# Optimization experiments

Measured on AMD Instinct MI355X. Metric: run time of the kernel, lower is better.

The kernel has to match this reference:

```python
import jax, jax.numpy as jnp
import numpy as np

N, E, H, HEADS, HD, L = 4096, 65536, 128, 4, 32, 4
NF, GF, EF, B = 16, 8, 4, 1


def _ln(x, g, b, eps=1e-5):
    mu = x.mean(-1, keepdims=True)
    v = ((x - mu) ** 2).mean(-1, keepdims=True)
    return (x - mu) * jax.lax.rsqrt(v + eps) * g + b


def _lin(x, W, b=None):
    y = x @ W.T
    return y if b is None else y + b


def _gelu(x):
    return jax.nn.gelu(x, approximate=False)


def setup_inputs() -> dict:
    key = jax.random.key(0)
    ks = iter(jax.random.split(key, 64))
    def rn(shape, s=0.05):
        return jax.random.normal(next(ks), shape, jnp.float32) * s
    inp = {}
    inp['x'] = jax.random.normal(next(ks), (N, NF), jnp.float32)
    inp['edge_index'] = jax.random.randint(next(ks), (2, E), 0, N, dtype=jnp.int32)
    inp['edge_attr'] = jax.random.normal(next(ks), (E, EF), jnp.float32)
    inp['u'] = jax.random.normal(next(ks), (1, GF), jnp.float32)
    inp['acting_mask'] = jax.random.randint(next(ks), (N,), 0, 2, dtype=jnp.int32).astype(bool)
    inp['h_tiles'] = jnp.zeros((N, H), jnp.float32)
    inp['batch'] = jnp.zeros((N,), jnp.int32)
    inp['turn_frac'] = jax.random.uniform(next(ks), (1,), jnp.float32)
    # node / global encoders
    inp['ne_W'] = rn((H, NF + 1)); inp['ne_b'] = jnp.zeros((H,)); inp['ne_g'] = jnp.ones((H,)); inp['ne_be'] = jnp.zeros((H,))
    inp['ge_W'] = rn((H, GF)); inp['ge_b'] = jnp.zeros((H,)); inp['ge_g'] = jnp.ones((H,)); inp['ge_be'] = jnp.zeros((H,))
    # GRUCell
    inp['gru_Wih'] = rn((3 * H, H)); inp['gru_bih'] = jnp.zeros((3 * H,))
    inp['gru_Whh'] = rn((3 * H, H)); inp['gru_bhh'] = jnp.zeros((3 * H,))
    # stacked GATv2 layers
    inp['gat_Wl'] = rn((L, H, H)); inp['gat_bl'] = jnp.zeros((L, H))
    inp['gat_Wr'] = rn((L, H, H)); inp['gat_br'] = jnp.zeros((L, H))
    inp['gat_We'] = rn((L, H, EF))
    inp['gat_att'] = rn((L, HEADS, HD))
    inp['gat_bias'] = jnp.zeros((L, H))
    inp['ln_g'] = jnp.ones((L, H)); inp['ln_b'] = jnp.zeros((L, H))
    # global MHA
    inp['attn_Win'] = rn((3 * H, H)); inp['attn_bin'] = jnp.zeros((3 * H,))
    inp['attn_Wout'] = rn((H, H)); inp['attn_bout'] = jnp.zeros((H,))
    inp['lng_g'] = jnp.ones((H,)); inp['lng_b'] = jnp.zeros((H,))
    # heads (edge_in = 2H + EF)
    inp['mv_W1'] = rn((H, 2 * H + EF)); inp['mv_b1'] = jnp.zeros((H,))
    inp['mv_W2'] = rn((1, H)); inp['mv_b2'] = jnp.zeros((1,))
    inp['fr_W1'] = rn((H, 2 * H + EF)); inp['fr_b1'] = jnp.zeros((H,))
    inp['fr_W2'] = rn((2, H)); inp['fr_b2'] = jnp.zeros((2,))
    inp['vl_W1'] = rn((H, 2 * H)); inp['vl_b1'] = jnp.zeros((H,))
    inp['vl_W2'] = rn((1, H)); inp['vl_b2'] = jnp.zeros((1,))
    return inp


def reference(x, edge_index, edge_attr, u, acting_mask, h_tiles, batch, turn_frac,
              ne_W, ne_b, ne_g, ne_be, ge_W, ge_b, ge_g, ge_be,
              gru_Wih, gru_bih, gru_Whh, gru_bhh,
              gat_Wl, gat_bl, gat_Wr, gat_br, gat_We, gat_att, gat_bias, ln_g, ln_b,
              attn_Win, attn_bin, attn_Wout, attn_bout, lng_g, lng_b,
              mv_W1, mv_b1, mv_W2, mv_b2, fr_W1, fr_b1, fr_W2, fr_b2,
              vl_W1, vl_b1, vl_W2, vl_b2):
    Nn = x.shape[0]
    src, dst = edge_index[0], edge_index[1]
    xa = jnp.concatenate([x, jnp.broadcast_to(turn_frac, (Nn, 1))], -1)
    h = _gelu(_ln(_lin(xa, ne_W, ne_b), ne_g, ne_be))
    ue = _gelu(_ln(_lin(u, ge_W, ge_b), ge_g, ge_be))
    h = h + ue[batch]
    # GRUCell (torch semantics)
    gi = _lin(h, gru_Wih, gru_bih)
    gh = _lin(h_tiles, gru_Whh, gru_bhh)
    i_r, i_z, i_n = jnp.split(gi, 3, -1)
    h_r, h_z, h_n = jnp.split(gh, 3, -1)
    r = jax.nn.sigmoid(i_r + h_r)
    z = jax.nn.sigmoid(i_z + h_z)
    n = jnp.tanh(i_n + r * h_n)
    h = (1.0 - z) * n + z * h_tiles
    h_tiles_new = jax.lax.stop_gradient(h)
    # stacked GATv2 message passing (eval mode: no dropout)
    for l in range(L):
        xl = _lin(h, gat_Wl[l], gat_bl[l]).reshape(Nn, HEADS, HD)   # source messages
        xr = _lin(h, gat_Wr[l], gat_br[l]).reshape(Nn, HEADS, HD)   # target
        ee = (edge_attr @ gat_We[l].T).reshape(-1, HEADS, HD)
        m = xl[src]                                                 # [E,heads,hd]
        s = jax.nn.leaky_relu(m + xr[dst] + ee, negative_slope=0.2)
        score = (s * gat_att[l]).sum(-1)                            # [E,heads]
        mx = jax.ops.segment_max(score, dst, num_segments=Nn)
        mx = jnp.where(jnp.isfinite(mx), mx, 0.0)
        ex = jnp.exp(score - mx[dst])
        den = jax.ops.segment_sum(ex, dst, num_segments=Nn)
        alpha_e = ex / (den[dst] + 1e-16)
        agg = jax.ops.segment_sum(alpha_e[..., None] * m, dst, num_segments=Nn)
        h_mp = agg.reshape(Nn, H) + gat_bias[l]
        h = _ln(h + h_mp, ln_g[l], ln_b[l])
    # global self-attention over all nodes as one sequence
    q, k, v = jnp.split(_lin(h, attn_Win, attn_bin), 3, -1)
    q = q.reshape(Nn, HEADS, HD); k = k.reshape(Nn, HEADS, HD); v = v.reshape(Nn, HEADS, HD)
    att = jax.nn.softmax(jnp.einsum('nhd,mhd->hnm', q, k) / np.float32(np.sqrt(HD)), axis=-1)
    ao = jnp.einsum('hnm,mhd->nhd', att, v).reshape(Nn, H)
    h = _ln(h + _lin(ao, attn_Wout, attn_bout), lng_g, lng_b)
    # edge heads
    eemb = jnp.concatenate([h[src], h[dst], edge_attr], -1)         # [E, 2H+EF]
    move_logits = _lin(_gelu(_lin(eemb, mv_W1, mv_b1)), mv_W2, mv_b2)[:, 0]
    fp = _lin(_gelu(_lin(eemb, fr_W1, fr_b1)), fr_W2, fr_b2)
    alpha = jax.nn.softplus(fp[:, 0]) + 1e-4
    beta = jax.nn.softplus(fp[:, 1]) + 1e-4
    # value head (global mean pool + masked acting pool)
    cnt = jax.ops.segment_sum(jnp.ones((Nn, 1), h.dtype), batch, num_segments=B)
    gpool = jax.ops.segment_sum(h, batch, num_segments=B) / cnt
    ah = jnp.where(acting_mask[:, None], h, 0.0)
    asum = jax.ops.segment_sum(ah, batch, num_segments=B) / cnt
    acnt = jnp.maximum(jax.ops.segment_sum(acting_mask[:, None].astype(h.dtype), batch, num_segments=B) / cnt, 1e-6)
    apool = asum / acnt
    vin = jnp.concatenate([gpool, apool], -1)
    value = _lin(_gelu(_lin(vin, vl_W1, vl_b1)), vl_W2, vl_b2)[:, 0]
    return move_logits, alpha, beta, value, h_tiles_new
```

## Files before the change

### kernel.cpp

```cpp
#include <hip/hip_runtime.h>
#include <math.h>


#define NN 4096
#define EE 65536
#define HH 128
#define NHEADS 4
#define HDIM 32
#define NLAYERS 4
#define NFEAT 16
#define GFEAT 8
#define EFEAT 4
#define KS 4
#define KPAD 296
#define XSTR 136
#define KSTR 40
#define VSTR 72

typedef short bf16x8 __attribute__((ext_vector_type(8)));
typedef float f32x4  __attribute__((ext_vector_type(4)));
union UB { uint4 u; bf16x8 v; };

__device__ __forceinline__ float gelu_f(float x){
  return 0.5f * x * (1.0f + erff(x * 0.7071067811865475f));
}
__device__ __forceinline__ float gelu_fast(float x){
  float u = 0.7978845608f * (x + 0.044715f * x * x * x);
  float t = __expf(-2.0f * fmaxf(u, -40.0f));
  float th = 1.0f - 2.0f * t / (1.0f + t);
  return 0.5f * x * (1.0f + th);
}
__device__ __forceinline__ float sigm_fast(float x){ return 1.0f / (1.0f + __expf(-x)); }
__device__ __forceinline__ float tanh_fast(float x){
  float t = __expf(-2.0f * fmaxf(x, -40.0f));
  return 1.0f - 2.0f * t / (1.0f + t);
}
__device__ __forceinline__ float softplus_f(float x){ return x > 20.0f ? x : log1pf(expf(x)); }
__device__ __forceinline__ unsigned short f2bf(float x){
  unsigned u = __float_as_uint(x);
  unsigned r = (u + 0x7FFFu + ((u >> 16) & 1u)) >> 16;
  return (unsigned short)r;
}
__device__ __forceinline__ float bf2f(unsigned short x){
  return __uint_as_float(((unsigned)x) << 16);
}
__device__ __forceinline__ unsigned pack2bf(float lo, float hi){
  unsigned a = (__float_as_uint(lo) + 0x8000u) >> 16;
  unsigned b = (__float_as_uint(hi) + 0x8000u) & 0xFFFF0000u;
  return a | b;
}

__device__ __forceinline__ float block_sum128(float v, float* red){
  int j = threadIdx.x;
  red[j] = v; __syncthreads();
  for (int s = 64; s > 0; s >>= 1){
    if (j < s) red[j] += red[j + s];
    __syncthreads();
  }
  float r = red[0];
  __syncthreads();
  return r;
}

__global__ void k_hist(const int* __restrict__ ei, int* __restrict__ cnt){
  int e = blockIdx.x * 256 + threadIdx.x;
  if (e < EE) atomicAdd(&cnt[ei[EE + e]], 1);
}

__global__ void k_scan(const int* __restrict__ cnt, int* __restrict__ off, int* __restrict__ cur){
  __shared__ int part[256];
  int t = threadIdx.x;
  int local[16];
  int s = 0;
  #pragma unroll
  for (int i = 0; i < 16; i++){ local[i] = s; s += cnt[t * 16 + i]; }
  part[t] = s; __syncthreads();
  for (int o = 1; o < 256; o <<= 1){
    int v = (t >= o) ? part[t - o] : 0;
    __syncthreads();
    part[t] += v;
    __syncthreads();
  }
  int base = part[t] - s;
  #pragma unroll
  for (int i = 0; i < 16; i++){ int o = base + local[i]; off[t * 16 + i] = o; cur[t * 16 + i] = o; }
  if (t == 255) off[NN] = part[255];
}

__global__ void k_scatter(const int* __restrict__ ei, int* __restrict__ cur,
                          int* __restrict__ srcs, int* __restrict__ rank){
  int e = blockIdx.x * 256 + threadIdx.x;
  if (e < EE){
    int d = ei[EE + e];
    int p = atomicAdd(&cur[d], 1);
    srcs[p] = ei[e];
    rank[e] = p;
  }
}

__global__ void k_wprep(const float* __restrict__ Wih, const float* __restrict__ Whh,
                        const float* __restrict__ Wl, const float* __restrict__ Wr,
                        const float* __restrict__ Win, const float* __restrict__ Wout,
                        const float* __restrict__ tiles,
                        const float* __restrict__ bl, const float* __restrict__ br,
                        const float* __restrict__ ea,
                        const float* __restrict__ mvW1, const float* __restrict__ frW1,
                        unsigned short* __restrict__ wbuf, unsigned short* __restrict__ tilesb,
                        float* __restrict__ blrc,
                        unsigned short* __restrict__ wbE, unsigned short* __restrict__ eab,
                        int* __restrict__ cnt, float* __restrict__ gsum){
  int i = blockIdx.x * 256 + threadIdx.x;
  if (i < 49152){ wbuf[i] = f2bf(Wih[i]); }
  else if (i < 98304){ int j = i - 49152; wbuf[49152 + j] = f2bf(Whh[j]); }
  else if (i < 229376){
    int j = i - 98304;
    int l = j >> 15, rem = j & 32767, m = rem >> 7, k = rem & 127;
    float v = (m < 128) ? Wl[l * 16384 + m * 128 + k] : Wr[l * 16384 + (m - 128) * 128 + k];
    wbuf[98304 + j] = f2bf(v);
  }
  else if (i < 278528){ int j = i - 229376; wbuf[229376 + j] = f2bf(Win[j]); }
  else if (i < 294912){ int j = i - 278528; wbuf[278528 + j] = f2bf(Wout[j]); }
  else if (i < 819200){ int j = i - 294912; tilesb[j] = f2bf(tiles[j]); }
  else if (i < 820224){
    int j = i - 819200;
    int l = j >> 8, m = j & 255;
    blrc[j] = (m < 128) ? bl[l * 128 + m] : br[l * 128 + m - 128];
  }
  else if (i < 896000){
    int j = i - 820224;
    int n = j / KPAD, k = j - n * KPAD;
    float v = 0.0f;
    if (k < 2 * HH + EFEAT) v = (n < HH) ? mvW1[n * (2 * HH + EFEAT) + k]
                                         : frW1[(n - HH) * (2 * HH + EFEAT) + k];
    wbE[j] = f2bf(v);
  }
  else if (i < 1158144){
    int j = i - 896000;
    eab[j] = f2bf(ea[j]);
  }
  else if (i < 1162240){ cnt[i - 1158144] = 0; }
  else if (i < 1162497){ gsum[i - 1162240] = 0.0f; }
}

__device__ __forceinline__ void gemm_core(const unsigned short* __restrict__ Xb, int n0,
                                          const unsigned short* __restrict__ Wb, int m0,
                                          unsigned short* Xs, f32x4 acc[8]){
  int t = threadIdx.x;
  #pragma unroll
  for (int k2 = 0; k2 < 4; k2++){
    int v = t + k2 * 256;
    int r = v >> 4, c8 = v & 15;
    *(uint4*)(Xs + r * XSTR + c8 * 8) = *(const uint4*)(Xb + (n0 + r) * 128 + c8 * 8);
  }
  __syncthreads();
  int ln = t & 63, w = t >> 6, lm = ln & 15, quad = ln >> 4;
  const unsigned short* abase = Xs + (16 * w + lm) * XSTR + quad * 8;
  const unsigned short* bbase = Wb + (m0 + lm) * 128 + quad * 8;
  UB af[4];
  #pragma unroll
  for (int ks = 0; ks < 4; ks++) af[ks].u = *(const uint4*)(abase + ks * 32);
  #pragma unroll
  for (int i = 0; i < 8; i++) acc[i] = (f32x4){0.f, 0.f, 0.f, 0.f};
  #pragma unroll
  for (int t2 = 0; t2 < 8; t2++){
    #pragma unroll
    for (int ks = 0; ks < 4; ks++){
      UB bu;
      bu.u = *(const uint4*)(bbase + t2 * 16 * 128 + ks * 32);
      acc[t2] = __builtin_amdgcn_mfma_f32_16x16x32_bf16(af[ks].v, bu.v, acc[t2], 0, 0, 0);
    }
  }
}

template<int MTOT>
__global__ __launch_bounds__(256) void k_lin(const unsigned short* __restrict__ Xb,
                                             const unsigned short* __restrict__ Wb,
                                             const float* __restrict__ bias,
                                             float* __restrict__ Y){
  __shared__ __align__(16) unsigned short Xs[64 * XSTR];
  int t = threadIdx.x;
  int n0 = blockIdx.x * 64, m0 = blockIdx.y * 128;
  f32x4 acc[8];
  gemm_core(Xb, n0, Wb, m0, Xs, acc);
  int ln = t & 63, w = t >> 6, lm = ln & 15, quad = ln >> 4;
  #pragma unroll
  for (int t2 = 0; t2 < 8; t2++){
    float bv = bias[m0 + t2 * 16 + lm];
    #pragma unroll
    for (int r = 0; r < 4; r++){
      Y[(n0 + 16 * w + quad * 4 + r) * MTOT + m0 + t2 * 16 + lm] = acc[t2][r] + bv;
    }
  }
}

__global__ __launch_bounds__(256) void k_gru_lin(const unsigned short* __restrict__ hb,
                                                 const unsigned short* __restrict__ tilesb,
                                                 const unsigned short* __restrict__ Wihb,
                                                 const unsigned short* __restrict__ Whhb,
                                                 const float* __restrict__ bih,
                                                 const float* __restrict__ bhh,
                                                 float* __restrict__ gi, float* __restrict__ gh){
  __shared__ __align__(16) unsigned short Xs[64 * XSTR];
  int z = blockIdx.z;
  const unsigned short* Xb = z ? tilesb : hb;
  const unsigned short* Wb = z ? Whhb : Wihb;
  const float* bias = z ? bhh : bih;
  float* Y = z ? gh : gi;
  int t = threadIdx.x;
  int n0 = blockIdx.x * 64, m0 = blockIdx.y * 128;
  f32x4 acc[8];
  gemm_core(Xb, n0, Wb, m0, Xs, acc);
  int ln = t & 63, w = t >> 6, lm = ln & 15, quad = ln >> 4;
  #pragma unroll
  for (int t2 = 0; t2 < 8; t2++){
    float bv = bias[m0 + t2 * 16 + lm];
    #pragma unroll
    for (int r = 0; r < 4; r++){
      Y[(n0 + 16 * w + quad * 4 + r) * 384 + m0 + t2 * 16 + lm] = acc[t2][r] + bv;
    }
  }
}

__global__ __launch_bounds__(256) void k_lin_gat(const unsigned short* __restrict__ Xb,
                                                 const unsigned short* __restrict__ Wb,
                                                 const float* __restrict__ bias,
                                                 unsigned short* __restrict__ Y,
                                                 float* __restrict__ den){
  __shared__ __align__(16) unsigned short Xs[64 * XSTR];
  int t = threadIdx.x;
  int gid = (blockIdx.y * gridDim.x + blockIdx.x) * 256 + t;
  if (gid < NN * NHEADS) den[gid] = 0.0f;
  int n0 = blockIdx.x * 64, m0 = blockIdx.y * 128;
  f32x4 acc[8];
  gemm_core(Xb, n0, Wb, m0, Xs, acc);
  int ln = t & 63, w = t >> 6, lm = ln & 15, quad = ln >> 4;
  #pragma unroll
  for (int t2 = 0; t2 < 8; t2++){
    float bv = bias[m0 + t2 * 16 + lm];
    #pragma unroll
    for (int r = 0; r < 4; r++){
      Y[(n0 + 16 * w + quad * 4 + r) * 256 + m0 + t2 * 16 + lm] = f2bf(acc[t2][r] + bv);
    }
  }
}

__global__ __launch_bounds__(256) void k_lin_qkv(const unsigned short* __restrict__ Xb,
                                                 const unsigned short* __restrict__ Wb,
                                                 const float* __restrict__ bias,
                                                 unsigned short* __restrict__ qb,
                                                 unsigned short* __restrict__ kb,
                                                 unsigned short* __restrict__ vt){
  __shared__ __align__(16) unsigned short Xs[64 * XSTR];
  int t = threadIdx.x;
  int n0 = blockIdx.x * 64, m0 = blockIdx.y * 128;
  f32x4 acc[8];
  gemm_core(Xb, n0, Wb, m0, Xs, acc);
  int ln = t & 63, w = t >> 6, lm = ln & 15, quad = ln >> 4;
  int nb = n0 + 16 * w + quad * 4;
  const float scale = 0.17677669529663687f;
  if (blockIdx.y == 0){
    #pragma unroll
    for (int t2 = 0; t2 < 8; t2++){
      int m = t2 * 16 + lm;
      float bv = bias[m];
      #pragma unroll
      for (int r = 0; r < 4; r++) qb[(nb + r) * HH + m] = f2bf(acc[t2][r] + bv);
    }
  } else if (blockIdx.y == 1){
    #pragma unroll
    for (int t2 = 0; t2 < 8; t2++){
      int m = t2 * 16 + lm;
      float bv = bias[128 + m];
      #pragma unroll
      for (int r = 0; r < 4; r++) kb[(nb + r) * HH + m] = f2bf((acc[t2][r] + bv) * scale);
    }
  } else {
    #pragma unroll
    for (int t2 = 0; t2 < 8; t2++){
      int m = t2 * 16 + lm;
      float bv = bias[256 + m];
      uint2 p;
      p.x = pack2bf(acc[t2][0] + bv, acc[t2][1] + bv);
      p.y = pack2bf(acc[t2][2] + bv, acc[t2][3] + bv);
      *(uint2*)(vt + m * NN + nb) = p;
    }
  }
}

__global__ void k_node_enc(const float* __restrict__ x, const float* __restrict__ tf,
                           const float* __restrict__ W, const float* __restrict__ b,
                           const float* __restrict__ g, const float* __restrict__ be,
                           const float* __restrict__ u, const float* __restrict__ geW,
                           const float* __restrict__ geb, const float* __restrict__ geg,
                           const float* __restrict__ gebe,
                           float* __restrict__ h, unsigned short* __restrict__ hb){
  __shared__ float red[128];
  __shared__ float xs[NFEAT + 1];
  __shared__ float us[GFEAT];
  int n = blockIdx.x, j = threadIdx.x;
  if (j < NFEAT) xs[j] = x[n * NFEAT + j];
  if (j == NFEAT) xs[NFEAT] = tf[0];
  if (j >= 32 && j < 32 + GFEAT) us[j - 32] = u[j - 32];
  __syncthreads();
  float ua = geb[j];
  #pragma unroll
  for (int k = 0; k < GFEAT; k++) ua += us[k] * geW[j * GFEAT + k];
  float umu = block_sum128(ua, red) * (1.0f / HH);
  float ud = ua - umu;
  float uvar = block_sum128(ud * ud, red) * (1.0f / HH);
  float uej = gelu_f(ud * rsqrtf(uvar + 1e-5f) * geg[j] + gebe[j]);
  float acc = b[j];
  #pragma unroll
  for (int k = 0; k < NFEAT + 1; k++) acc += xs[k] * W[j * (NFEAT + 1) + k];
  float mu = block_sum128(acc, red) * (1.0f / HH);
  float d = acc - mu;
  float var = block_sum128(d * d, red) * (1.0f / HH);
  float r = gelu_f(d * rsqrtf(var + 1e-5f) * g[j] + be[j]) + uej;
  h[n * HH + j] = r;
  hb[n * HH + j] = f2bf(r);
}

__global__ void k_gru_comb(const float* __restrict__ gi, const float* __restrict__ gh,
                           const float* __restrict__ tiles, float* __restrict__ h,
                           unsigned short* __restrict__ hb, float* __restrict__ out_tiles){
  int idx = blockIdx.x * 256 + threadIdx.x;
  int n = idx >> 7, j = idx & 127;
  float ir = gi[n * 384 + j], iz = gi[n * 384 + 128 + j], inn = gi[n * 384 + 256 + j];
  float hr = gh[n * 384 + j], hz = gh[n * 384 + 128 + j], hn = gh[n * 384 + 256 + j];
  float r = sigm_fast(ir + hr), z = sigm_fast(iz + hz);
  float nn2 = tanh_fast(inn + r * hn);
  float ts = tiles[idx];
  float hnew = (1.0f - z) * nn2 + z * ts;
  h[idx] = hnew;
  hb[idx] = f2bf(hnew);
  out_tiles[idx] = hnew;
}

__global__ __launch_bounds__(256) void k_score(const int* __restrict__ ei, const float* __restrict__ ea,
                        const unsigned short* __restrict__ xlrb,
                        const float* __restrict__ We, const float* __restrict__ att,
                        const int* __restrict__ rank,
                        float* __restrict__ exs, float* __restrict__ den){
  __shared__ float4 We4[128];
  __shared__ float atts[128];
  int t = threadIdx.x;
  if (t < 128){ We4[t] = ((const float4*)We)[t]; atts[t] = att[t]; }
  __syncthreads();
  int el = t >> 4, g = t & 15;
  int e = blockIdx.x * 16 + el;
  int s = ei[e], d = ei[EE + e];
  float4 a = *(const float4*)(ea + e * 4);
  UB xlu, xru;
  xlu.u = *(const uint4*)(xlrb + s * 256 + g * 8);
  xru.u = *(const uint4*)(xlrb + d * 256 + 128 + g * 8);
  float sc = 0.0f;
  #pragma unroll
  for (int i = 0; i < 8; i++){
    int j = g * 8 + i;
    float4 w = We4[j];
    float v = bf2f((unsigned short)xlu.v[i]) + bf2f((unsigned short)xru.v[i])
            + a.x * w.x + a.y * w.y + a.z * w.z + a.w * w.w;
    v = v > 0.0f ? v : 0.2f * v;
    sc += v * atts[j];
  }
  sc += __shfl_xor(sc, 1);
  sc += __shfl_xor(sc, 2);
  if ((g & 3) == 0){
    float ev = __expf(sc);
    exs[rank[e] * 4 + (g >> 2)] = ev;
    atomicAdd(&den[d * 4 + (g >> 2)], ev);
  }
}

__global__ void k_aggln(const unsigned short* __restrict__ xlrb, const float* __restrict__ exs,
                        const float* __restrict__ den,
                        const int* __restrict__ off, const int* __restrict__ srcs,
                        const float* __restrict__ bias, const float* __restrict__ g,
                        const float* __restrict__ b, float* __restrict__ h,
                        unsigned short* __restrict__ hb){
  __shared__ float red[128];
  int n = blockIdx.x, j = threadIdx.x;
  int p0 = off[n], p1 = off[n + 1];
  int hh = j >> 5;
  float dinv = 1.0f / (den[n * 4 + hh] + 1e-16f);
  float agg = 0.0f;
  int p = p0;
  for (; p + 4 <= p1; p += 4){
    int s0 = srcs[p], s1 = srcs[p + 1], s2 = srcs[p + 2], s3 = srcs[p + 3];
    float w0 = exs[p * 4 + hh],       w1 = exs[(p + 1) * 4 + hh];
    float w2 = exs[(p + 2) * 4 + hh], w3 = exs[(p + 3) * 4 + hh];
    float x0 = bf2f(xlrb[s0 * 256 + j]);
    float x1 = bf2f(xlrb[s1 * 256 + j]);
    float x2 = bf2f(xlrb[s2 * 256 + j]);
    float x3 = bf2f(xlrb[s3 * 256 + j]);
    agg += w0 * x0 + w1 * x1 + w2 * x2 + w3 * x3;
  }
  for (; p < p1; p++){
    agg += exs[p * 4 + hh] * bf2f(xlrb[srcs[p] * 256 + j]);
  }
  agg *= dinv;
  float val = h[n * HH + j] + agg + bias[j];
  float mu = block_sum128(val, red) * (1.0f / HH);
  float d2 = val - mu;
  float var = block_sum128(d2 * d2, red) * (1.0f / HH);
  float r = d2 * rsqrtf(var + 1e-5f) * g[j] + b[j];
  h[n * HH + j] = r;
  hb[n * HH + j] = f2bf(r);
}

__global__ __launch_bounds__(256, 4) void k_attn_flash(
    const unsigned short* __restrict__ qb, const unsigned short* __restrict__ kb,
    const unsigned short* __restrict__ vt,
    float* __restrict__ pden, float* __restrict__ pacc){
  __shared__ __align__(16) unsigned short Kls[2][64 * KSTR];
  __shared__ __align__(16) unsigned short Vls[2][32 * VSTR];
  int t = threadIdx.x, w = t >> 6, ln = t & 63;
  int c = ln & 15, qd = ln >> 4;
  int hh = blockIdx.y, ks = blockIdx.z;
  int q0 = blockIdx.x * 64 + w * 16;
  UB qf; qf.u = *(const uint4*)(qb + (q0 + c) * HH + hh * HDIM + qd * 8);
  f32x4 o0a = {0,0,0,0}, o1a = {0,0,0,0}, o0b = {0,0,0,0}, o1b = {0,0,0,0};
  float denp = 0.f;
  int srcA = c + ((qd & 1) << 5);
  int srcB = srcA + 16;
  bool hi = qd >= 2;
  int kk = t >> 2, kp = t & 3;
  int vr = t >> 3, vc = t & 7;
  const unsigned short* kg = kb + hh * HDIM + kp * 8;
  const unsigned short* vg = vt + (hh * HDIM + vr) * NN + vc * 8;

  auto comp = [&](int buf, int hs, f32x4& O0, f32x4& O1){
    UB kf0, kf1, vf0, vf1, pt;
    kf0.u = *(const uint4*)(&Kls[buf][(hs * 32 + c) * KSTR + qd * 8]);
    kf1.u = *(const uint4*)(&Kls[buf][(hs * 32 + 16 + c) * KSTR + qd * 8]);
    vf0.u = *(const uint4*)(&Vls[buf][c * VSTR + hs * 32 + qd * 8]);
    vf1.u = *(const uint4*)(&Vls[buf][(16 + c) * VSTR + hs * 32 + qd * 8]);
    f32x4 s0 = {0,0,0,0}, s1 = {0,0,0,0};
    s0 = __builtin_amdgcn_mfma_f32_16x16x32_bf16(kf0.v, qf.v, s0, 0, 0, 0);
    s1 = __builtin_amdgcn_mfma_f32_16x16x32_bf16(kf1.v, qf.v, s1, 0, 0, 0);
    float e00 = __expf(s0[0]), e01 = __expf(s0[1]), e02 = __expf(s0[2]), e03 = __expf(s0[3]);
    float e10 = __expf(s1[0]), e11 = __expf(s1[1]), e12 = __expf(s1[2]), e13 = __expf(s1[3]);
    denp += (e00 + e01) + (e02 + e03) + (e10 + e11) + (e12 + e13);
    int p00 = (int)pack2bf(e00, e01), p01 = (int)pack2bf(e02, e03);
    int p10 = (int)pack2bf(e10, e11), p11 = (int)pack2bf(e12, e13);
    int a00 = __shfl(p00, srcA), a01 = __shfl(p01, srcA);
    int b00 = __shfl(p00, srcB), b01 = __shfl(p01, srcB);
    int a10 = __shfl(p10, srcA), a11 = __shfl(p11, srcA);
    int b10 = __shfl(p10, srcB), b11 = __shfl(p11, srcB);
    pt.u.x = (unsigned)(hi ? a10 : a00);
    pt.u.y = (unsigned)(hi ? a11 : a01);
    pt.u.z = (unsigned)(hi ? b10 : b00);
    pt.u.w = (unsigned)(hi ? b11 : b01);
    O0 = __builtin_amdgcn_mfma_f32_16x16x32_bf16(vf0.v, pt.v, O0, 0, 0, 0);
    O1 = __builtin_amdgcn_mfma_f32_16x16x32_bf16(vf1.v, pt.v, O1, 0, 0, 0);
  };

  const int kbeg = ks * (NN / KS);
  const int NIT = (NN / KS) / 64;
  {
    uint4 kr = *(const uint4*)(kg + (kbeg + kk) * HH);
    uint4 vr4 = *(const uint4*)(vg + kbeg);
    *(uint4*)(&Kls[0][kk * KSTR + kp * 8]) = kr;
    *(uint4*)(&Vls[0][vr * VSTR + vc * 8]) = vr4;
  }
  __syncthreads();
  for (int it = 0; it < NIT; it++){
    int buf = it & 1;
    if (it + 1 < NIT){
      int kn = kbeg + (it + 1) * 64;
      uint4 kr = *(const uint4*)(kg + (kn + kk) * HH);
      uint4 vr4 = *(const uint4*)(vg + kn);
      comp(buf, 0, o0a, o1a);
      comp(buf, 1, o0b, o1b);
      *(uint4*)(&Kls[buf ^ 1][kk * KSTR + kp * 8]) = kr;
      *(uint4*)(&Vls[buf ^ 1][vr * VSTR + vc * 8]) = vr4;
    } else {
      comp(buf, 0, o0a, o1a);
      comp(buf, 1, o0b, o1b);
    }
    __syncthreads();
  }

  f32x4 o0 = o0a + o0b, o1 = o1a + o1b;
  denp += __shfl_xor(denp, 16);
  denp += __shfl_xor(denp, 32);
  int pi = ((q0 + c) * NHEADS + hh) * KS + ks;
  if (qd == 0) pden[pi] = denp;
  #pragma unroll
  for (int r = 0; r < 4; r++){
    pacc[pi * HDIM + qd * 4 + r]      = o0[r];
    pacc[pi * HDIM + 16 + qd * 4 + r] = o1[r];
  }
}

__global__ __launch_bounds__(256) void k_attn_out(
    const float* __restrict__ pden, const float* __restrict__ pacc,
    const unsigned short* __restrict__ Wb, const float* __restrict__ bout,
    const float* __restrict__ g, const float* __restrict__ b,
    float* __restrict__ h, unsigned short* __restrict__ hb){
  __shared__ __align__(16) unsigned short Xs[64 * XSTR];
  int t = threadIdx.x;
  int n0 = blockIdx.x * 64;
  for (int idx = t; idx < 64 * 128; idx += 256){
    int r = idx >> 7, j = idx & 127;
    int n = n0 + r, hh = j >> 5, d = j & 31;
    float ds = 0.f, as = 0.f;
    #pragma unroll
    for (int ks2 = 0; ks2 < KS; ks2++){
      int pi = (n * NHEADS + hh) * KS + ks2;
      ds += pden[pi];
      as += pacc[pi * HDIM + d];
    }
    Xs[r * XSTR + j] = f2bf(as / ds);
  }
  __syncthreads();
  int ln = t & 63, w = t >> 6, lm = ln & 15, quad = ln >> 4;
  const unsigned short* abase = Xs + (16 * w + lm) * XSTR + quad * 8;
  const unsigned short* bbase = Wb + lm * 128 + quad * 8;
  UB af[4];
  #pragma unroll
  for (int ks2 = 0; ks2 < 4; ks2++) af[ks2].u = *(const uint4*)(abase + ks2 * 32);
  f32x4 acc[8];
  #pragma unroll
  for (int i = 0; i < 8; i++) acc[i] = (f32x4){0.f, 0.f, 0.f, 0.f};
  #pragma unroll
  for (int t2 = 0; t2 < 8; t2++){
    #pragma unroll
    for (int ks2 = 0; ks2 < 4; ks2++){
      UB bu;
      bu.u = *(const uint4*)(bbase + t2 * 16 * 128 + ks2 * 32);
      acc[t2] = __builtin_amdgcn_mfma_f32_16x16x32_bf16(af[ks2].v, bu.v, acc[t2], 0, 0, 0);
    }
  }
  int nb = n0 + 16 * w + quad * 4;
  float val[8][4];
  #pragma unroll
  for (int t2 = 0; t2 < 8; t2++){
    int m = t2 * 16 + lm;
    float bv = bout[m];
    #pragma unroll
    for (int r = 0; r < 4; r++)
      val[t2][r] = acc[t2][r] + bv + h[(nb + r) * HH + m];
  }
  float mu[4], rs[4];
  #pragma unroll
  for (int r = 0; r < 4; r++){
    float s = 0.f;
    #pragma unroll
    for (int t2 = 0; t2 < 8; t2++) s += val[t2][r];
    s += __shfl_xor(s, 1); s += __shfl_xor(s, 2);
    s += __shfl_xor(s, 4); s += __shfl_xor(s, 8);
    mu[r] = s * (1.0f / HH);
  }
  #pragma unroll
  for (int r = 0; r < 4; r++){
    float s = 0.f;
    #pragma unroll
    for (int t2 = 0; t2 < 8; t2++){ float d2 = val[t2][r] - mu[r]; s += d2 * d2; }
    s += __shfl_xor(s, 1); s += __shfl_xor(s, 2);
    s += __shfl_xor(s, 4); s += __shfl_xor(s, 8);
    rs[r] = rsqrtf(s * (1.0f / HH) + 1e-5f);
  }
  #pragma unroll
  for (int t2 = 0; t2 < 8; t2++){
    int m = t2 * 16 + lm;
    float gm = g[m], bm = b[m];
    #pragma unroll
    for (int r = 0; r < 4; r++){
      float o = (val[t2][r] - mu[r]) * rs[r] * gm + bm;
      h[(nb + r) * HH + m] = o;
      hb[(nb + r) * HH + m] = f2bf(o);
    }
  }
}

__global__ __launch_bounds__(256) void k_edge_mfma(
    const unsigned short* __restrict__ hb, const unsigned short* __restrict__ eab,
    const int* __restrict__ ei, const unsigned short* __restrict__ wb,
    const float* __restrict__ mvb1, const float* __restrict__ frb1,
    const float* __restrict__ mvW2, const float* __restrict__ mvb2,
    const float* __restrict__ frW2, const float* __restrict__ frb2,
    float* __restrict__ out){
  __shared__ __align__(16) unsigned short As[64 * KPAD];
  __shared__ float am[64], a0[64], a1[64];
  int t = threadIdx.x;
  int e0 = blockIdx.x * 64;
  if (t < 64){ am[t] = 0.f; a0[t] = 0.f; a1[t] = 0.f; }
  {
    int el = t >> 2, p = t & 3;
    int e = e0 + el;
    int node = (p < 2) ? ei[e] : ei[EE + e];
    int half = p & 1;
    const uint4* srcp = (const uint4*)(hb + node * HH + half * 64);
    uint4* dstp = (uint4*)(As + el * KPAD + (p >> 1) * 128 + half * 64);
    #pragma unroll
    for (int i = 0; i < 8; i++) dstp[i] = srcp[i];
    if (p == 0){
      unsigned short* tail = As + el * KPAD + 256;
      tail[0] = eab[e * 4];     tail[1] = eab[e * 4 + 1];
      tail[2] = eab[e * 4 + 2]; tail[3] = eab[e * 4 + 3];
      #pragma unroll
      for (int i = 4; i < KPAD - 256; i++) tail[i] = 0;
    }
  }
  int ln = t & 63, w = t >> 6, lm = ln & 15, quad = ln >> 4;
  const unsigned short* bbase = wb + (w * 64 + lm) * KPAD + quad * 8;
  f32x4 acc[4][4];
  #pragma unroll
  for (int rt = 0; rt < 4; rt++)
    #pragma unroll
    for (int t2 = 0; t2 < 4; t2++) acc[rt][t2] = (f32x4){0.f, 0.f, 0.f, 0.f};
  __syncthreads();
  for (int ks = 0; ks < 9; ks++){
    UB bf[4], af[4];
    #pragma unroll
    for (int t2 = 0; t2 < 4; t2++) bf[t2].u = *(const uint4*)(bbase + t2 * 16 * KPAD + ks * 32);
    #pragma unroll
    for (int rt = 0; rt < 4; rt++) af[rt].u = *(const uint4*)(As + (16 * rt + lm) * KPAD + quad * 8 + ks * 32);
    #pragma unroll
    for (int rt = 0; rt < 4; rt++)
      #pragma unroll
      for (int t2 = 0; t2 < 4; t2++)
        acc[rt][t2] = __builtin_amdgcn_mfma_f32_16x16x32_bf16(af[rt].v, bf[t2].v, acc[rt][t2], 0, 0, 0);
  }
  if (w < 2){
    #pragma unroll
    for (int rt = 0; rt < 4; rt++){
      #pragma unroll
      for (int r = 0; r < 4; r++){
        float s = 0.f;
        #pragma unroll
        for (int t2 = 0; t2 < 4; t2++){
          int n = w * 64 + t2 * 16 + lm;
          s += gelu_fast(acc[rt][t2][r] + mvb1[n]) * mvW2[n];
        }
        #pragma unroll
        for (int d = 1; d < 16; d <<= 1) s += __shfl_xor(s, d);
        if (lm == 0) atomicAdd(&am[16 * rt + 4 * quad + r], s);
      }
    }
  } else {
    #pragma unroll
    for (int rt = 0; rt < 4; rt++){
      #pragma unroll
      for (int r = 0; r < 4; r++){
        float s0 = 0.f, s1 = 0.f;
        #pragma unroll
        for (int t2 = 0; t2 < 4; t2++){
          int n = (w - 2) * 64 + t2 * 16 + lm;
          float g = gelu_fast(acc[rt][t2][r] + frb1[n]);
          s0 += g * frW2[n];
          s1 += g * frW2[128 + n];
        }
        #pragma unroll
        for (int d = 1; d < 16; d <<= 1){ s0 += __shfl_xor(s0, d); s1 += __shfl_xor(s1, d); }
        if (lm == 0){
          atomicAdd(&a0[16 * rt + 4 * quad + r], s0);
          atomicAdd(&a1[16 * rt + 4 * quad + r], s1);
        }
      }
    }
  }
  __syncthreads();
  if (t < 64){
    int e = e0 + t;
    out[e]          = am[t] + mvb2[0];
    out[EE + e]     = softplus_f(a0[t] + frb2[0]) + 1e-4f;
    out[2 * EE + e] = softplus_f(a1[t] + frb2[1]) + 1e-4f;
  }
}

__global__ void k_pool(const float* __restrict__ h, const unsigned char* __restrict__ mask,
                       float* __restrict__ gsum, float* __restrict__ msum, float* __restrict__ mcnt){
  int bb = blockIdx.x, j = threadIdx.x;
  float ga = 0.0f, ma = 0.0f;
  int n0 = bb * 32;
  for (int i = 0; i < 32; i++){
    int n = n0 + i;
    float v = h[n * HH + j];
    ga += v;
    if (mask[n]) ma += v;
  }
  atomicAdd(&gsum[j], ga);
  atomicAdd(&msum[j], ma);
  if (j == 0){
    float c = 0.0f;
    for (int i = 0; i < 32; i++) c += mask[n0 + i] ? 1.0f : 0.0f;
    atomicAdd(mcnt, c);
  }
}

__global__ void k_value(const float* __restrict__ gsum, const float* __restrict__ msum,
                        const float* __restrict__ mcnt,
                        const float* __restrict__ W1, const float* __restrict__ b1,
                        const float* __restrict__ W2, const float* __restrict__ b2,
                        float* __restrict__ out_val){
  __shared__ float red[128];
  __shared__ float vin[256];
  int j = threadIdx.x;
  float gp = gsum[j] * (1.0f / NN);
  float as = msum[j] * (1.0f / NN);
  float ac = fmaxf(mcnt[0] * (1.0f / NN), 1e-6f);
  vin[j] = gp; vin[HH + j] = as / ac;
  __syncthreads();
  float acc = b1[j];
  const float* w = &W1[j * 256];
  #pragma unroll 4
  for (int k = 0; k < 256; k++) acc += vin[k] * w[k];
  float hv = gelu_f(acc) * W2[j];
  float s = block_sum128(hv, red);
  if (j == 0) out_val[0] = s + b2[0];
}

extern "C" void kernel_launch(void* const* d_in, const int* in_sizes, int n_in,
                              void* d_out, int out_size, void* d_ws, size_t ws_size,
                              hipStream_t stream){
  (void)in_sizes; (void)n_in; (void)out_size; (void)ws_size;
  const float* x        = (const float*)d_in[0];
  const int*   ei       = (const int*)d_in[1];
  const float* ea       = (const float*)d_in[2];
  const float* u        = (const float*)d_in[3];
  const unsigned char* mask = (const unsigned char*)d_in[4];
  const float* tiles    = (const float*)d_in[5];
  const float* tf       = (const float*)d_in[7];
  const float* ne_W  = (const float*)d_in[8];
  const float* ne_b  = (const float*)d_in[9];
  const float* ne_g  = (const float*)d_in[10];
  const float* ne_be = (const float*)d_in[11];
  const float* ge_W  = (const float*)d_in[12];
  const float* ge_b  = (const float*)d_in[13];
  const float* ge_g  = (const float*)d_in[14];
  const float* ge_be = (const float*)d_in[15];
  const float* gru_Wih = (const float*)d_in[16];
  const float* gru_bih = (const float*)d_in[17];
  const float* gru_Whh = (const float*)d_in[18];
  const float* gru_bhh = (const float*)d_in[19];
  const float* gat_Wl  = (const float*)d_in[20];
  const float* gat_bl  = (const float*)d_in[21];
  const float* gat_Wr  = (const float*)d_in[22];
  const float* gat_br  = (const float*)d_in[23];
  const float* gat_We  = (const float*)d_in[24];
  const float* gat_att = (const float*)d_in[25];
  const float* gat_bias= (const float*)d_in[26];
  const float* ln_g    = (const float*)d_in[27];
  const float* ln_b    = (const float*)d_in[28];
  const float* attn_Win = (const float*)d_in[29];
  const float* attn_bin = (const float*)d_in[30];
  const float* attn_Wout= (const float*)d_in[31];
  const float* attn_bout= (const float*)d_in[32];
  const float* lng_g    = (const float*)d_in[33];
  const float* lng_b    = (const float*)d_in[34];
  const float* mv_W1 = (const float*)d_in[35];
  const float* mv_b1 = (const float*)d_in[36];
  const float* mv_W2 = (const float*)d_in[37];
  const float* mv_b2 = (const float*)d_in[38];
  const float* fr_W1 = (const float*)d_in[39];
  const float* fr_b1 = (const float*)d_in[40];
  const float* fr_W2 = (const float*)d_in[41];
  const float* fr_b2 = (const float*)d_in[42];
  const float* vl_W1 = (const float*)d_in[43];
  const float* vl_b1 = (const float*)d_in[44];
  const float* vl_W2 = (const float*)d_in[45];
  const float* vl_b2 = (const float*)d_in[46];

  float* ws = (float*)d_ws;
  float* h      = ws;
  float* xlr    = ws + 524288;
  unsigned short* hb     = (unsigned short*)(ws + 1572864);
  unsigned short* tilesb = (unsigned short*)(ws + 1835008);
  unsigned short* wbuf   = (unsigned short*)(ws + 2097152);
  unsigned short* Wihb  = wbuf;
  unsigned short* Whhb  = wbuf + 49152;
  unsigned short* Wlrb  = wbuf + 98304;
  unsigned short* Winb  = wbuf + 229376;
  unsigned short* Woutb = wbuf + 278528;
  float* blrc   = ws + 2244608;
  float* gsum   = ws + 2245760;
  float* msum   = ws + 2245888;
  float* mcnt   = ws + 2246016;
  int*   cnt    = (int*)(ws + 2246032);
  int*   off    = cnt + NN;
  int*   cur    = off + NN + 1;
  unsigned short* eab = (unsigned short*)(ws + 2323904);
  unsigned short* wbE = (unsigned short*)(ws + 2454976);
  float* S      = ws + 2492864;
  float* gi = S;
  float* gh = S + 1572864;
  float* exs = S;
  int*   srcs = (int*)(S + 262144);
  int*   rank = (int*)(S + 327680);
  unsigned short* xlrb = (unsigned short*)xlr;
  float* den = xlr + 524288;
  unsigned short* qb = (unsigned short*)xlr;
  unsigned short* kb = (unsigned short*)(xlr + 262144);
  unsigned short* vt = (unsigned short*)(xlr + 524288 + 16384);
  float* pacc = S;
  float* pden = S + 2097152;

  float* out       = (float*)d_out;
  float* out_val   = out + 3 * EE;
  float* out_tiles = out + 3 * EE + 1;

  k_wprep<<<(1162497 + 255) / 256, 256, 0, stream>>>(gru_Wih, gru_Whh, gat_Wl, gat_Wr,
                                                     attn_Win, attn_Wout, tiles,
                                                     gat_bl, gat_br, ea, mv_W1, fr_W1,
                                                     wbuf, tilesb, blrc, wbE, eab,
                                                     cnt, gsum);

  k_node_enc<<<NN, 128, 0, stream>>>(x, tf, ne_W, ne_b, ne_g, ne_be,
                                     u, ge_W, ge_b, ge_g, ge_be, h, hb);

  { dim3 g(NN / 64, 3, 2);
    k_gru_lin<<<g, 256, 0, stream>>>(hb, tilesb, Wihb, Whhb, gru_bih, gru_bhh, gi, gh); }
  k_gru_comb<<<NN * HH / 256, 256, 0, stream>>>(gi, gh, tiles, h, hb, out_tiles);

  k_hist   <<<EE / 256, 256, 0, stream>>>(ei, cnt);
  k_scan   <<<1, 256, 0, stream>>>(cnt, off, cur);
  k_scatter<<<EE / 256, 256, 0, stream>>>(ei, cur, srcs, rank);

  for (int l = 0; l < NLAYERS; l++){
    { dim3 g(NN / 64, 2);
      k_lin_gat<<<g, 256, 0, stream>>>(hb, Wlrb + l * 32768, blrc + l * 256, xlrb, den); }
    k_score<<<EE / 16, 256, 0, stream>>>(ei, ea, xlrb,
                                         gat_We + l * HH * EFEAT,
                                         gat_att + l * NHEADS * HDIM, rank, exs, den);
    k_aggln<<<NN, 128, 0, stream>>>(xlrb, exs, den, off, srcs,
                                    gat_bias + l * HH, ln_g + l * HH, ln_b + l * HH, h, hb);
  }

  { dim3 g(NN / 64, 3);
    k_lin_qkv<<<g, 256, 0, stream>>>(hb, Winb, attn_bin, qb, kb, vt); }
  { dim3 gattn(NN / 64, NHEADS, KS);
    k_attn_flash<<<gattn, 256, 0, stream>>>(qb, kb, vt, pden, pacc); }
  k_attn_out<<<NN / 64, 256, 0, stream>>>(pden, pacc, Woutb, attn_bout, lng_g, lng_b, h, hb);

  k_edge_mfma<<<EE / 64, 256, 0, stream>>>(hb, eab, ei, wbE, mv_b1, fr_b1,
                                           mv_W2, mv_b2, fr_W2, fr_b2, out);

  k_pool <<<128, 128, 0, stream>>>(h, mask, gsum, msum, mcnt);
  k_value<<<1, 128, 0, stream>>>(gsum, msum, mcnt, vl_W1, vl_b1, vl_W2, vl_b2, out_val);
}
```

Baseline: 410.6 us.

## Fuse pooling into attention output, simplify gelu, tune edge kernel

Moves the global and masked-node pooling into the attention-output layernorm epilogue, reducing per-column sums in shared memory and atomically adding them to global accumulators, so the separate pool kernel and its re-read of h go away. The tanh-form gelu is rewritten as x*sigmoid(1.5958*u), which needs fewer operations. The edge MLP kernel gets a min-blocks launch bound and a fully unrolled K loop. An unused linear kernel template is deleted. The extra atomics in the fused epilogue and the register pressure from the edge kernel bound are the main costs traded in.

```diff
diff --git a/kernel.cpp b/kernel.cpp
--- a/kernel.cpp
+++ b/kernel.cpp
@@ -25,10 +25,9 @@
   return 0.5f * x * (1.0f + erff(x * 0.7071067811865475f));
 }
 __device__ __forceinline__ float gelu_fast(float x){
-  float u = 0.7978845608f * (x + 0.044715f * x * x * x);
-  float t = __expf(-2.0f * fmaxf(u, -40.0f));
-  float th = 1.0f - 2.0f * t / (1.0f + t);
-  return 0.5f * x * (1.0f + th);
+  float u = x + 0.044715f * x * x * x;
+  float t = __expf(-1.5957691216f * u);
+  return x / (1.0f + t);
 }
 __device__ __forceinline__ float sigm_fast(float x){ return 1.0f / (1.0f + __expf(-x)); }
 __device__ __forceinline__ float tanh_fast(float x){
@@ -168,27 +167,6 @@
       UB bu;
       bu.u = *(const uint4*)(bbase + t2 * 16 * 128 + ks * 32);
       acc[t2] = __builtin_amdgcn_mfma_f32_16x16x32_bf16(af[ks].v, bu.v, acc[t2], 0, 0, 0);
-    }
-  }
-}
-
-template<int MTOT>
-__global__ __launch_bounds__(256) void k_lin(const unsigned short* __restrict__ Xb,
-                                             const unsigned short* __restrict__ Wb,
-                                             const float* __restrict__ bias,
-                                             float* __restrict__ Y){
-  __shared__ __align__(16) unsigned short Xs[64 * XSTR];
-  int t = threadIdx.x;
-  int n0 = blockIdx.x * 64, m0 = blockIdx.y * 128;
-  f32x4 acc[8];
-  gemm_core(Xb, n0, Wb, m0, Xs, acc);
-  int ln = t & 63, w = t >> 6, lm = ln & 15, quad = ln >> 4;
-  #pragma unroll
-  for (int t2 = 0; t2 < 8; t2++){
-    float bv = bias[m0 + t2 * 16 + lm];
-    #pragma unroll
-    for (int r = 0; r < 4; r++){
-      Y[(n0 + 16 * w + quad * 4 + r) * MTOT + m0 + t2 * 16 + lm] = acc[t2][r] + bv;
     }
   }
 }
@@ -497,10 +475,15 @@
     const float* __restrict__ pden, const float* __restrict__ pacc,
     const unsigned short* __restrict__ Wb, const float* __restrict__ bout,
     const float* __restrict__ g, const float* __restrict__ b,
-    float* __restrict__ h, unsigned short* __restrict__ hb){
+    const unsigned char* __restrict__ mask,
+    float* __restrict__ h, unsigned short* __restrict__ hb,
+    float* __restrict__ gsum, float* __restrict__ msum, float* __restrict__ mcnt){
   __shared__ __align__(16) unsigned short Xs[64 * XSTR];
+  __shared__ float colg[128], colm[128], colc;
   int t = threadIdx.x;
   int n0 = blockIdx.x * 64;
+  if (t < 128){ colg[t] = 0.f; colm[t] = 0.f; }
+  if (t == 128) colc = 0.f;
   for (int idx = t; idx < 64 * 128; idx += 256){
     int r = idx >> 7, j = idx & 127;
     int n = n0 + r, hh = j >> 5, d = j & 31;
@@ -561,20 +544,41 @@
     s += __shfl_xor(s, 4); s += __shfl_xor(s, 8);
     rs[r] = rsqrtf(s * (1.0f / HH) + 1e-5f);
   }
+  uchar4 mk = *(const uchar4*)(mask + nb);
+  float mkf[4] = { mk.x ? 1.f : 0.f, mk.y ? 1.f : 0.f, mk.z ? 1.f : 0.f, mk.w ? 1.f : 0.f };
   #pragma unroll
   for (int t2 = 0; t2 < 8; t2++){
     int m = t2 * 16 + lm;
     float gm = g[m], bm = b[m];
+    float sg = 0.f, sm = 0.f;
     #pragma unroll
     for (int r = 0; r < 4; r++){
       float o = (val[t2][r] - mu[r]) * rs[r] * gm + bm;
       h[(nb + r) * HH + m] = o;
       hb[(nb + r) * HH + m] = f2bf(o);
-    }
-  }
-}
-
-__global__ __launch_bounds__(256) void k_edge_mfma(
+      sg += o;
+      sm += mkf[r] * o;
+    }
+    sg += __shfl_xor(sg, 16); sg += __shfl_xor(sg, 32);
+    sm += __shfl_xor(sm, 16); sm += __shfl_xor(sm, 32);
+    if (quad == 0){
+      atomicAdd(&colg[m], sg);
+      atomicAdd(&colm[m], sm);
+    }
+  }
+  if (lm == 0){
+    float c = mkf[0] + mkf[1] + mkf[2] + mkf[3];
+    atomicAdd(&colc, c);
+  }
+  __syncthreads();
+  if (t < 128){
+    atomicAdd(&gsum[t], colg[t]);
+    atomicAdd(&msum[t], colm[t]);
+  }
+  if (t == 128) atomicAdd(mcnt, colc);
+}
+
+__global__ __launch_bounds__(256, 4) void k_edge_mfma(
     const unsigned short* __restrict__ hb, const unsigned short* __restrict__ eab,
     const int* __restrict__ ei, const unsigned short* __restrict__ wb,
     const float* __restrict__ mvb1, const float* __restrict__ frb1,
@@ -611,6 +615,7 @@
     #pragma unroll
     for (int t2 = 0; t2 < 4; t2++) acc[rt][t2] = (f32x4){0.f, 0.f, 0.f, 0.f};
   __syncthreads();
+  #pragma unroll
   for (int ks = 0; ks < 9; ks++){
     UB bf[4], af[4];
     #pragma unroll
@@ -667,26 +672,6 @@
     out[e]          = am[t] + mvb2[0];
     out[EE + e]     = softplus_f(a0[t] + frb2[0]) + 1e-4f;
     out[2 * EE + e] = softplus_f(a1[t] + frb2[1]) + 1e-4f;
-  }
-}
-
-__global__ void k_pool(const float* __restrict__ h, const unsigned char* __restrict__ mask,
-                       float* __restrict__ gsum, float* __restrict__ msum, float* __restrict__ mcnt){
-  int bb = blockIdx.x, j = threadIdx.x;
-  float ga = 0.0f, ma = 0.0f;
-  int n0 = bb * 32;
-  for (int i = 0; i < 32; i++){
-    int n = n0 + i;
-    float v = h[n * HH + j];
-    ga += v;
-    if (mask[n]) ma += v;
-  }
-  atomicAdd(&gsum[j], ga);
-  atomicAdd(&msum[j], ma);
-  if (j == 0){
-    float c = 0.0f;
-    for (int i = 0; i < 32; i++) c += mask[n0 + i] ? 1.0f : 0.0f;
-    atomicAdd(mcnt, c);
   }
 }
 
@@ -832,11 +817,11 @@
     k_lin_qkv<<<g, 256, 0, stream>>>(hb, Winb, attn_bin, qb, kb, vt); }
   { dim3 gattn(NN / 64, NHEADS, KS);
     k_attn_flash<<<gattn, 256, 0, stream>>>(qb, kb, vt, pden, pacc); }
-  k_attn_out<<<NN / 64, 256, 0, stream>>>(pden, pacc, Woutb, attn_bout, lng_g, lng_b, h, hb);
+  k_attn_out<<<NN / 64, 256, 0, stream>>>(pden, pacc, Woutb, attn_bout, lng_g, lng_b,
+                                          mask, h, hb, gsum, msum, mcnt);
 
   k_edge_mfma<<<EE / 64, 256, 0, stream>>>(hb, eab, ei, wbE, mv_b1, fr_b1,
                                            mv_W2, mv_b2, fr_W2, fr_b2, out);
 
-  k_pool <<<128, 128, 0, stream>>>(h, mask, gsum, msum, mcnt);
   k_value<<<1, 128, 0, stream>>>(gsum, msum, mcnt, vl_W1, vl_b1, vl_W2, vl_b2, out_val);
 }
```

New measurement: 397.2 us. -3.3%, faster.
